# Kernel optimization log

Hardware: AMD Instinct MI355X
Metric: run time of the kernel (lower is better)

Reference implementation:

```python
import jax, jax.numpy as jnp
import numpy as np

N = 100000
E = 1600000
IN_C = 128
OUT_C = 64


def setup_inputs() -> dict:
    key = jax.random.key(0)
    ks = jax.random.split(key, 8)
    x = jax.random.normal(ks[0], (N, IN_C), dtype=jnp.float32)
    edge_index = jax.random.randint(ks[1], (2, E), 0, N, dtype=jnp.int64)
    neg_edge_index = jax.random.randint(ks[2], (2, E), 0, N, dtype=jnp.int64)
    # GCNConv params (glorot-ish init)
    W = jax.random.normal(ks[3], (IN_C, OUT_C), dtype=jnp.float32) / np.sqrt(IN_C)
    b = jnp.zeros((OUT_C,), dtype=jnp.float32)
    # classifier Linear(2*out_channels, 2)
    Wc = jax.random.normal(ks[4], (2 * OUT_C, 2), dtype=jnp.float32) / np.sqrt(2 * OUT_C)
    bc = jnp.zeros((2,), dtype=jnp.float32)
    return {"x": x, "edge_index": edge_index, "neg_edge_index": neg_edge_index,
            "W": W, "b": b, "Wc": Wc, "bc": bc}


def gcn_conv(x, edge_index, W, b):
    # Add self-loops, symmetric normalization: D^{-1/2} (A+I) D^{-1/2} X W + b
    loops = jnp.arange(N, dtype=edge_index.dtype)
    src = jnp.concatenate([edge_index[0], loops])  # [E+N]
    dst = jnp.concatenate([edge_index[1], loops])  # [E+N]
    deg = jax.ops.segment_sum(jnp.ones_like(dst, dtype=x.dtype), dst, num_segments=N)
    dinv = jax.lax.rsqrt(jnp.maximum(deg, 1e-12))
    norm = dinv[src] * dinv[dst]                   # [E+N]
    xw = x @ W                                     # [N, OUT_C] transform first (cheaper)
    msg = norm[:, None] * xw[src]                  # gather + scale
    out = jax.ops.segment_sum(msg, dst, num_segments=N)  # scatter-add aggregate
    return out + b


def reference(x, edge_index, neg_edge_index, W, b, Wc, bc):
    h = jax.nn.relu(gcn_conv(x, edge_index, W, b))           # [N, OUT_C]
    total = jnp.concatenate([edge_index, neg_edge_index], axis=1)  # [2, 2E]
    edge_feat = jnp.concatenate([h[total[0]], h[total[1]]], axis=1)  # [2E, 2*OUT_C]
    return edge_feat @ Wc + bc                               # [2E, 2]
```

## Files before the change

### kernel.cpp

```cpp
#include <hip/hip_runtime.h>

#define N_NODES 100000
#define N_EDGES 1600000
#define IN_C    128
#define OUT_C   64

#define SB_NODES 1024
#define NSB  ((N_NODES + SB_NODES - 1) / SB_NODES)
#define SCAP 17408
#define ACHUNK 8192
#define NABLK ((N_EDGES + ACHUNK - 1) / ACHUNK)

__device__ inline unsigned pack_bf16x2(float lo, float hi) {
    unsigned a = __float_as_uint(lo), b2 = __float_as_uint(hi);
    a  += 0x7fff + ((a  >> 16) & 1);
    b2 += 0x7fff + ((b2 >> 16) & 1);
    return (a >> 16) | (b2 & 0xffff0000u);
}
__device__ inline float bf_lo(unsigned v) { return __uint_as_float(v << 16); }
__device__ inline float bf_hi(unsigned v) { return __uint_as_float(v & 0xffff0000u); }

__global__ void zero_kernel(int* __restrict__ cursor) {
    int i = blockIdx.x * blockDim.x + threadIdx.x;
    if (i < NSB) cursor[i] = 0;
}

__global__ __launch_bounds__(256) void sorta_kernel(const int* __restrict__ ei,
                                                    int* __restrict__ cursor,
                                                    int* __restrict__ sb) {
    __shared__ int hist[NSB];
    __shared__ int base_[NSB];
    __shared__ int cur[NSB];
    const int t = threadIdx.x;
    const long long e0 = (long long)blockIdx.x * ACHUNK;
    if (t < NSB) { hist[t] = 0; cur[t] = 0; }
    __syncthreads();
    const int* dsts = ei + N_EDGES;
#pragma unroll
    for (int k = 0; k < ACHUNK / 1024; ++k) {
        long long i4 = e0 / 4 + t + k * 256;
        if (i4 * 4 + 3 < N_EDGES) {
            int4 d = *(const int4*)&dsts[i4 * 4];
            atomicAdd(&hist[d.x >> 10], 1);
            atomicAdd(&hist[d.y >> 10], 1);
            atomicAdd(&hist[d.z >> 10], 1);
            atomicAdd(&hist[d.w >> 10], 1);
        }
    }
    __syncthreads();
    if (t < NSB) {
        int c = hist[t];
        base_[t] = c ? atomicAdd(&cursor[t], c) : 0;
    }
    __syncthreads();
#pragma unroll
    for (int k = 0; k < ACHUNK / 1024; ++k) {
        long long i4 = e0 / 4 + t + k * 256;
        if (i4 * 4 + 3 < N_EDGES) {
            int4 s4 = *(const int4*)&ei[i4 * 4];
            int4 d4 = *(const int4*)&dsts[i4 * 4];
            int sv[4] = {s4.x, s4.y, s4.z, s4.w};
            int dv[4] = {d4.x, d4.y, d4.z, d4.w};
#pragma unroll
            for (int j = 0; j < 4; ++j) {
                int bk = dv[j] >> 10;
                int pos = base_[bk] + atomicAdd(&cur[bk], 1);
                if (pos < SCAP)
                    sb[bk * SCAP + pos] = sv[j] * SB_NODES + (dv[j] & (SB_NODES - 1));
            }
        }
    }
}

__global__ __launch_bounds__(256) void sortb_kernel(const int* __restrict__ cursor,
                                                    int* __restrict__ sb,
                                                    float* __restrict__ dinv,
                                                    int* __restrict__ rowbeg,
                                                    int* __restrict__ rowend) {
    __shared__ int hist[SB_NODES];
    __shared__ int pref[SB_NODES + 1];
    __shared__ int cur[SB_NODES];
    __shared__ int sc[256];
    __shared__ int sorted[SCAP];
    const int t = threadIdx.x, b = blockIdx.x;
    for (int k = t; k < SB_NODES; k += 256) { hist[k] = 0; cur[k] = 0; }
    __syncthreads();
    int m = cursor[b]; if (m > SCAP) m = SCAP;
    int* bb = sb + b * SCAP;
    for (int i = t; i < m; i += 256) atomicAdd(&hist[bb[i] & (SB_NODES - 1)], 1);
    __syncthreads();
    int c0 = hist[4 * t], c1 = hist[4 * t + 1], c2 = hist[4 * t + 2], c3 = hist[4 * t + 3];
    int tsum = c0 + c1 + c2 + c3;
    sc[t] = tsum;
    __syncthreads();
    for (int off = 1; off < 256; off <<= 1) {
        int u = (t >= off) ? sc[t - off] : 0;
        __syncthreads();
        sc[t] += u;
        __syncthreads();
    }
    int excl = sc[t] - tsum;
    pref[4 * t]     = excl;
    pref[4 * t + 1] = excl + c0;
    pref[4 * t + 2] = excl + c0 + c1;
    pref[4 * t + 3] = excl + c0 + c1 + c2;
    if (t == 255) pref[SB_NODES] = sc[255];
    __syncthreads();
    for (int i = t; i < m; i += 256) {
        int e = bb[i];
        int dl = e & (SB_NODES - 1);
        int pos = pref[dl] + atomicAdd(&cur[dl], 1);
        sorted[pos] = e >> 10;
    }
    __syncthreads();
    for (int i = t; i < m; i += 256) bb[i] = sorted[i];
    for (int k = t; k < SB_NODES; k += 256) {
        int n = b * SB_NODES + k;
        if (n < N_NODES) {
            rowbeg[n] = b * SCAP + pref[k];
            rowend[n] = b * SCAP + pref[k + 1];
            dinv[n]   = rsqrtf((float)hist[k] + 1.0f);
        }
    }
}

#define XN  32
#define SXS 132
__global__ __launch_bounds__(256) void xws_kernel(const float* __restrict__ x,
                                                  const float* __restrict__ W,
                                                  const float* __restrict__ dinv,
                                                  unsigned* __restrict__ xwsh) {
    __shared__ float sW[IN_C * OUT_C];
    __shared__ float sx[XN * SXS];
    const int t = threadIdx.x;
    const int n0 = blockIdx.x * XN;
    const float4* W4 = (const float4*)W;
    float4* sW4 = (float4*)sW;
#pragma unroll
    for (int k = 0; k < 8; ++k) sW4[t + k * 256] = W4[t + k * 256];
#pragma unroll
    for (int k = 0; k < 4; ++k) {
        int idx = (t + k * 256) * 4;
        int r = idx >> 7, kk = idx & 127;
        int n = n0 + r;
        float4 v = (n < N_NODES) ? *(const float4*)&x[(long long)n * IN_C + kk]
                                 : make_float4(0.f, 0.f, 0.f, 0.f);
        *(float4*)&sx[r * SXS + kk] = v;
    }
    __syncthreads();
    const int r  = t >> 4;
    const int cq = (t & 15) << 2;
    float4 a0 = make_float4(0.f,0.f,0.f,0.f), a1 = a0;
#pragma unroll 8
    for (int k = 0; k < IN_C; ++k) {
        float x0 = sx[r * SXS + k];
        float x1 = sx[(r + 16) * SXS + k];
        float4 wv = *(const float4*)&sW[(k << 6) + cq];
        a0.x = fmaf(x0, wv.x, a0.x); a0.y = fmaf(x0, wv.y, a0.y);
        a0.z = fmaf(x0, wv.z, a0.z); a0.w = fmaf(x0, wv.w, a0.w);
        a1.x = fmaf(x1, wv.x, a1.x); a1.y = fmaf(x1, wv.y, a1.y);
        a1.z = fmaf(x1, wv.z, a1.z); a1.w = fmaf(x1, wv.w, a1.w);
    }
    int na = n0 + r, nb = n0 + r + 16;
    if (na < N_NODES) {
        float di = dinv[na];
        uint2 o = make_uint2(pack_bf16x2(a0.x * di, a0.y * di),
                             pack_bf16x2(a0.z * di, a0.w * di));
        *(uint2*)&xwsh[(long long)na * 32 + ((t & 15) << 1)] = o;
    }
    if (nb < N_NODES) {
        float di = dinv[nb];
        uint2 o = make_uint2(pack_bf16x2(a1.x * di, a1.y * di),
                             pack_bf16x2(a1.z * di, a1.w * di));
        *(uint2*)&xwsh[(long long)nb * 32 + ((t & 15) << 1)] = o;
    }
}

__global__ __launch_bounds__(256) void aggnode_kernel(
    const int* __restrict__ rowbeg, const int* __restrict__ rowend,
    const int* __restrict__ srcs, const float* __restrict__ dinv,
    const unsigned* __restrict__ xwsh, const float* __restrict__ b,
    const float* __restrict__ Wc, const float* __restrict__ bc,
    float4* __restrict__ pq) {
    const int lane = threadIdx.x & 63;
    const int node = blockIdx.x * 4 + (threadIdx.x >> 6);
    if (node >= N_NODES) return;
    const int beg = rowbeg[node], end = rowend[node];
    const int half = lane >> 5, hl = lane & 31;
    float ax0 = 0.f, ay0 = 0.f, ax1 = 0.f, ay1 = 0.f;
    float ax2 = 0.f, ay2 = 0.f, ax3 = 0.f, ay3 = 0.f;
    for (int i = beg; i < end; i += 64) {
        int cnt = end - i;
        if (cnt > 64) cnt = 64;
        int sv = (lane < cnt) ? srcs[i + lane] : 0;
        int j = 0;
        for (; j + 15 < cnt; j += 16) {
#pragma unroll
            for (int u = 0; u < 8; ++u) {
                int s = __shfl(sv, j + 2 * u + half);
                unsigned v = xwsh[s * 32 + hl];
                float lo = bf_lo(v), hi = bf_hi(v);
                if (u == 0 || u == 4) { ax0 += lo; ay0 += hi; }
                else if (u == 1 || u == 5) { ax1 += lo; ay1 += hi; }
                else if (u == 2 || u == 6) { ax2 += lo; ay2 += hi; }
                else { ax3 += lo; ay3 += hi; }
            }
        }
        for (; j + 1 < cnt; j += 2) {
            int s = __shfl(sv, j + half);
            unsigned v = xwsh[s * 32 + hl];
            ax0 += bf_lo(v); ay0 += bf_hi(v);
        }
        if (j < cnt) {
            int s = __shfl(sv, j);
            if (lane < 32) {
                unsigned v = xwsh[s * 32 + hl];
                ax1 += bf_lo(v); ay1 += bf_hi(v);
            }
        }
    }
    float ax = (ax0 + ax1) + (ax2 + ax3);
    float ay = (ay0 + ay1) + (ay2 + ay3);
    ax += __shfl(ax, lane + 32);
    ay += __shfl(ay, lane + 32);
    unsigned vs = xwsh[node * 32 + hl];
    ax += bf_lo(vs); ay += bf_hi(vs);
    float di = dinv[node];
    float2 b2 = ((const float2*)b)[hl];
    float h0 = fmaxf(fmaf(di, ax, b2.x), 0.f);
    float h1 = fmaxf(fmaf(di, ay, b2.y), 0.f);
    float4 wcs = ((const float4*)Wc)[hl];
    float4 wcd = ((const float4*)(Wc + 2 * OUT_C))[hl];
    float p0 = h0 * wcs.x + h1 * wcs.z;
    float p1 = h0 * wcs.y + h1 * wcs.w;
    float q0 = h0 * wcd.x + h1 * wcd.z;
    float q1 = h0 * wcd.y + h1 * wcd.w;
#pragma unroll
    for (int off = 16; off; off >>= 1) {
        p0 += __shfl_down(p0, off); p1 += __shfl_down(p1, off);
        q0 += __shfl_down(q0, off); q1 += __shfl_down(q1, off);
    }
    if (lane == 0) pq[node] = make_float4(p0 + bc[0], p1 + bc[1], q0, q1);
}

__global__ void edge_kernel(const int* __restrict__ ei, const int* __restrict__ nei,
                            const float4* __restrict__ pq, float4* __restrict__ out4) {
    int idx = blockIdx.x * blockDim.x + threadIdx.x;
    if (idx >= N_EDGES) return;
    int e2 = idx * 2;
    int2 ss, dd;
    if (e2 < N_EDGES) {
        ss = *(const int2*)&ei[e2];
        dd = *(const int2*)&ei[N_EDGES + e2];
    } else {
        int f = e2 - N_EDGES;
        ss = *(const int2*)&nei[f];
        dd = *(const int2*)&nei[N_EDGES + f];
    }
    float4 pa = pq[ss.x], qa = pq[dd.x];
    float4 pb = pq[ss.y], qb = pq[dd.y];
    out4[idx] = make_float4(pa.x + qa.z, pa.y + qa.w, pb.x + qb.z, pb.y + qb.w);
}

extern "C" void kernel_launch(void* const* d_in, const int* in_sizes, int n_in,
                              void* d_out, int out_size, void* d_ws, size_t ws_size,
                              hipStream_t stream) {
    const float* x   = (const float*)d_in[0];
    const int*   ei  = (const int*)  d_in[1];
    const int*   nei = (const int*)  d_in[2];
    const float* W   = (const float*)d_in[3];
    const float* b   = (const float*)d_in[4];
    const float* Wc  = (const float*)d_in[5];
    const float* bc  = (const float*)d_in[6];

    int*      wsI    = (int*)d_ws;
    float*    dinv   = (float*)wsI;
    unsigned* xwsh   = (unsigned*)(wsI + 100352);
    float*    pq     = (float*)(wsI + 3300352);
    int*      cursor = wsI + 3700352;
    int*      rowbeg = wsI + 3700480;
    int*      rowend = wsI + 3800832;
    int*      sbuf   = wsI + 3901184;

    const int B = 256;
    zero_kernel<<<1, B, 0, stream>>>(cursor);
    sorta_kernel<<<NABLK, B, 0, stream>>>(ei, cursor, sbuf);
    sortb_kernel<<<NSB, B, 0, stream>>>(cursor, sbuf, dinv, rowbeg, rowend);
    xws_kernel<<<(N_NODES + XN - 1) / XN, B, 0, stream>>>(x, W, dinv, xwsh);
    aggnode_kernel<<<(N_NODES + 3) / 4, B, 0, stream>>>(rowbeg, rowend, sbuf, dinv,
                                                        xwsh, b, Wc, bc, (float4*)pq);
    edge_kernel<<<(N_EDGES + B - 1) / B, B, 0, stream>>>(ei, nei, (const float4*)pq,
                                                         (float4*)d_out);
}
```

Measured before the change: 270.6 us.

## Shrink sort buckets, per-wave histograms, scalar-indexed aggregation, split p/q arrays

Halves the coarse sort bucket size to 512 nodes with smaller chunks and capacity, and gives each wave its own shared histogram in the first sort pass to reduce atomic contention. The aggregation kernel now reads neighbour indices as wave-uniform scalar loads instead of a vector load plus shuffles, and takes a uniform node index via readfirstlane. Node scores are split into separate p and q float2 arrays, and the edge kernel handles four edges per thread with int4 index loads. The smaller SCAP leaves less headroom against bucket overflow, which would silently drop edges.

```diff
diff --git a/kernel.cpp b/kernel.cpp
--- a/kernel.cpp
+++ b/kernel.cpp
@@ -5,10 +5,10 @@
 #define IN_C    128
 #define OUT_C   64
 
-#define SB_NODES 1024
+#define SB_NODES 512
 #define NSB  ((N_NODES + SB_NODES - 1) / SB_NODES)
-#define SCAP 17408
-#define ACHUNK 8192
+#define SCAP 9216
+#define ACHUNK 4096
 #define NABLK ((N_EDGES + ACHUNK - 1) / ACHUNK)
 
 __device__ inline unsigned pack_bf16x2(float lo, float hi) {
@@ -28,12 +28,12 @@
 __global__ __launch_bounds__(256) void sorta_kernel(const int* __restrict__ ei,
                                                     int* __restrict__ cursor,
                                                     int* __restrict__ sb) {
-    __shared__ int hist[NSB];
+    __shared__ int histW[4][NSB];
     __shared__ int base_[NSB];
     __shared__ int cur[NSB];
-    const int t = threadIdx.x;
+    const int t = threadIdx.x, w = t >> 6;
     const long long e0 = (long long)blockIdx.x * ACHUNK;
-    if (t < NSB) { hist[t] = 0; cur[t] = 0; }
+    for (int i = t; i < 4 * NSB; i += 256) (&histW[0][0])[i] = 0;
     __syncthreads();
     const int* dsts = ei + N_EDGES;
 #pragma unroll
@@ -41,16 +41,17 @@
         long long i4 = e0 / 4 + t + k * 256;
         if (i4 * 4 + 3 < N_EDGES) {
             int4 d = *(const int4*)&dsts[i4 * 4];
-            atomicAdd(&hist[d.x >> 10], 1);
-            atomicAdd(&hist[d.y >> 10], 1);
-            atomicAdd(&hist[d.z >> 10], 1);
-            atomicAdd(&hist[d.w >> 10], 1);
+            atomicAdd(&histW[w][d.x >> 9], 1);
+            atomicAdd(&histW[w][d.y >> 9], 1);
+            atomicAdd(&histW[w][d.z >> 9], 1);
+            atomicAdd(&histW[w][d.w >> 9], 1);
         }
     }
     __syncthreads();
     if (t < NSB) {
-        int c = hist[t];
+        int c = histW[0][t] + histW[1][t] + histW[2][t] + histW[3][t];
         base_[t] = c ? atomicAdd(&cursor[t], c) : 0;
+        cur[t] = 0;
     }
     __syncthreads();
 #pragma unroll
@@ -63,7 +64,7 @@
             int dv[4] = {d4.x, d4.y, d4.z, d4.w};
 #pragma unroll
             for (int j = 0; j < 4; ++j) {
-                int bk = dv[j] >> 10;
+                int bk = dv[j] >> 9;
                 int pos = base_[bk] + atomicAdd(&cur[bk], 1);
                 if (pos < SCAP)
                     sb[bk * SCAP + pos] = sv[j] * SB_NODES + (dv[j] & (SB_NODES - 1));
@@ -89,8 +90,8 @@
     int* bb = sb + b * SCAP;
     for (int i = t; i < m; i += 256) atomicAdd(&hist[bb[i] & (SB_NODES - 1)], 1);
     __syncthreads();
-    int c0 = hist[4 * t], c1 = hist[4 * t + 1], c2 = hist[4 * t + 2], c3 = hist[4 * t + 3];
-    int tsum = c0 + c1 + c2 + c3;
+    int c0 = hist[2 * t], c1 = hist[2 * t + 1];
+    int tsum = c0 + c1;
     sc[t] = tsum;
     __syncthreads();
     for (int off = 1; off < 256; off <<= 1) {
@@ -100,17 +101,15 @@
         __syncthreads();
     }
     int excl = sc[t] - tsum;
-    pref[4 * t]     = excl;
-    pref[4 * t + 1] = excl + c0;
-    pref[4 * t + 2] = excl + c0 + c1;
-    pref[4 * t + 3] = excl + c0 + c1 + c2;
+    pref[2 * t]     = excl;
+    pref[2 * t + 1] = excl + c0;
     if (t == 255) pref[SB_NODES] = sc[255];
     __syncthreads();
     for (int i = t; i < m; i += 256) {
         int e = bb[i];
         int dl = e & (SB_NODES - 1);
         int pos = pref[dl] + atomicAdd(&cur[dl], 1);
-        sorted[pos] = e >> 10;
+        sorted[pos] = e >> 9;
     }
     __syncthreads();
     for (int i = t; i < m; i += 256) bb[i] = sorted[i];
@@ -181,48 +180,40 @@
     const int* __restrict__ srcs, const float* __restrict__ dinv,
     const unsigned* __restrict__ xwsh, const float* __restrict__ b,
     const float* __restrict__ Wc, const float* __restrict__ bc,
-    float4* __restrict__ pq) {
+    float2* __restrict__ p, float2* __restrict__ q) {
     const int lane = threadIdx.x & 63;
-    const int node = blockIdx.x * 4 + (threadIdx.x >> 6);
-    if (node >= N_NODES) return;
+    int node = __builtin_amdgcn_readfirstlane(blockIdx.x * 4 + (threadIdx.x >> 6));
     const int beg = rowbeg[node], end = rowend[node];
     const int half = lane >> 5, hl = lane & 31;
     float ax0 = 0.f, ay0 = 0.f, ax1 = 0.f, ay1 = 0.f;
     float ax2 = 0.f, ay2 = 0.f, ax3 = 0.f, ay3 = 0.f;
-    for (int i = beg; i < end; i += 64) {
-        int cnt = end - i;
-        if (cnt > 64) cnt = 64;
-        int sv = (lane < cnt) ? srcs[i + lane] : 0;
-        int j = 0;
-        for (; j + 15 < cnt; j += 16) {
-#pragma unroll
-            for (int u = 0; u < 8; ++u) {
-                int s = __shfl(sv, j + 2 * u + half);
-                unsigned v = xwsh[s * 32 + hl];
-                float lo = bf_lo(v), hi = bf_hi(v);
-                if (u == 0 || u == 4) { ax0 += lo; ay0 += hi; }
-                else if (u == 1 || u == 5) { ax1 += lo; ay1 += hi; }
-                else if (u == 2 || u == 6) { ax2 += lo; ay2 += hi; }
-                else { ax3 += lo; ay3 += hi; }
-            }
-        }
-        for (; j + 1 < cnt; j += 2) {
-            int s = __shfl(sv, j + half);
-            unsigned v = xwsh[s * 32 + hl];
-            ax0 += bf_lo(v); ay0 += bf_hi(v);
-        }
-        if (j < cnt) {
-            int s = __shfl(sv, j);
-            if (lane < 32) {
-                unsigned v = xwsh[s * 32 + hl];
-                ax1 += bf_lo(v); ay1 += bf_hi(v);
-            }
-        }
+    int i = beg;
+    for (; i + 7 < end; i += 8) {
+        int s0 = srcs[i + 0], s1 = srcs[i + 1], s2 = srcs[i + 2], s3 = srcs[i + 3];
+        int s4 = srcs[i + 4], s5 = srcs[i + 5], s6 = srcs[i + 6], s7 = srcs[i + 7];
+        unsigned v0 = xwsh[(half ? s1 : s0) * 32 + hl];
+        unsigned v1 = xwsh[(half ? s3 : s2) * 32 + hl];
+        unsigned v2 = xwsh[(half ? s5 : s4) * 32 + hl];
+        unsigned v3 = xwsh[(half ? s7 : s6) * 32 + hl];
+        ax0 += bf_lo(v0); ay0 += bf_hi(v0);
+        ax1 += bf_lo(v1); ay1 += bf_hi(v1);
+        ax2 += bf_lo(v2); ay2 += bf_hi(v2);
+        ax3 += bf_lo(v3); ay3 += bf_hi(v3);
+    }
+    for (; i + 1 < end; i += 2) {
+        int sa = srcs[i], sb2 = srcs[i + 1];
+        unsigned v = xwsh[(half ? sb2 : sa) * 32 + hl];
+        ax0 += bf_lo(v); ay0 += bf_hi(v);
+    }
+    if (i < end) {
+        int s = srcs[i];
+        unsigned v = xwsh[s * 32 + hl];
+        if (!half) { ax1 += bf_lo(v); ay1 += bf_hi(v); }
     }
     float ax = (ax0 + ax1) + (ax2 + ax3);
     float ay = (ay0 + ay1) + (ay2 + ay3);
-    ax += __shfl(ax, lane + 32);
-    ay += __shfl(ay, lane + 32);
+    ax += __shfl(ax, hl + 32);
+    ay += __shfl(ay, hl + 32);
     unsigned vs = xwsh[node * 32 + hl];
     ax += bf_lo(vs); ay += bf_hi(vs);
     float di = dinv[node];
@@ -240,26 +231,30 @@
         p0 += __shfl_down(p0, off); p1 += __shfl_down(p1, off);
         q0 += __shfl_down(q0, off); q1 += __shfl_down(q1, off);
     }
-    if (lane == 0) pq[node] = make_float4(p0 + bc[0], p1 + bc[1], q0, q1);
+    if (lane == 0) {
+        p[node] = make_float2(p0 + bc[0], p1 + bc[1]);
+        q[node] = make_float2(q0, q1);
+    }
 }
 
 __global__ void edge_kernel(const int* __restrict__ ei, const int* __restrict__ nei,
-                            const float4* __restrict__ pq, float4* __restrict__ out4) {
+                            const float2* __restrict__ p, const float2* __restrict__ q,
+                            float4* __restrict__ out4) {
     int idx = blockIdx.x * blockDim.x + threadIdx.x;
-    if (idx >= N_EDGES) return;
-    int e2 = idx * 2;
-    int2 ss, dd;
-    if (e2 < N_EDGES) {
-        ss = *(const int2*)&ei[e2];
-        dd = *(const int2*)&ei[N_EDGES + e2];
-    } else {
-        int f = e2 - N_EDGES;
-        ss = *(const int2*)&nei[f];
-        dd = *(const int2*)&nei[N_EDGES + f];
-    }
-    float4 pa = pq[ss.x], qa = pq[dd.x];
-    float4 pb = pq[ss.y], qb = pq[dd.y];
-    out4[idx] = make_float4(pa.x + qa.z, pa.y + qa.w, pb.x + qb.z, pb.y + qb.w);
+    if (idx >= 2 * N_EDGES / 4) return;
+    int e4 = idx * 4;
+    const int *S, *D;
+    int off;
+    if (e4 < N_EDGES) { S = ei;  D = ei  + N_EDGES; off = e4; }
+    else              { S = nei; D = nei + N_EDGES; off = e4 - N_EDGES; }
+    int4 s4 = *(const int4*)&S[off];
+    int4 d4 = *(const int4*)&D[off];
+    float2 pa = p[s4.x], qa = q[d4.x];
+    float2 pb = p[s4.y], qb = q[d4.y];
+    float2 pc = p[s4.z], qc = q[d4.z];
+    float2 pd = p[s4.w], qd = q[d4.w];
+    out4[idx * 2]     = make_float4(pa.x + qa.x, pa.y + qa.y, pb.x + qb.x, pb.y + qb.y);
+    out4[idx * 2 + 1] = make_float4(pc.x + qc.x, pc.y + qc.y, pd.x + qd.x, pd.y + qd.y);
 }
 
 extern "C" void kernel_launch(void* const* d_in, const int* in_sizes, int n_in,
@@ -276,19 +271,20 @@
     int*      wsI    = (int*)d_ws;
     float*    dinv   = (float*)wsI;
     unsigned* xwsh   = (unsigned*)(wsI + 100352);
-    float*    pq     = (float*)(wsI + 3300352);
-    int*      cursor = wsI + 3700352;
-    int*      rowbeg = wsI + 3700480;
-    int*      rowend = wsI + 3800832;
-    int*      sbuf   = wsI + 3901184;
+    float*    p      = (float*)(wsI + 3300352);
+    float*    q      = (float*)(wsI + 3501056);
+    int*      cursor = wsI + 3701760;
+    int*      rowbeg = wsI + 3702016;
+    int*      rowend = wsI + 3802368;
+    int*      sbuf   = wsI + 3902720;
 
     const int B = 256;
     zero_kernel<<<1, B, 0, stream>>>(cursor);
     sorta_kernel<<<NABLK, B, 0, stream>>>(ei, cursor, sbuf);
     sortb_kernel<<<NSB, B, 0, stream>>>(cursor, sbuf, dinv, rowbeg, rowend);
     xws_kernel<<<(N_NODES + XN - 1) / XN, B, 0, stream>>>(x, W, dinv, xwsh);
-    aggnode_kernel<<<(N_NODES + 3) / 4, B, 0, stream>>>(rowbeg, rowend, sbuf, dinv,
-                                                        xwsh, b, Wc, bc, (float4*)pq);
-    edge_kernel<<<(N_EDGES + B - 1) / B, B, 0, stream>>>(ei, nei, (const float4*)pq,
-                                                         (float4*)d_out);
-}
+    aggnode_kernel<<<N_NODES / 4, B, 0, stream>>>(rowbeg, rowend, sbuf, dinv, xwsh,
+                                                  b, Wc, bc, (float2*)p, (float2*)q);
+    edge_kernel<<<(2 * N_EDGES / 4 + B - 1) / B, B, 0, stream>>>(
+        ei, nei, (const float2*)p, (const float2*)q, (float4*)d_out);
+}
```

Result: faster. 254.6 us (-5.9%).
